# Kernel tuning notes

Measured on AMD Instinct MI355X. Metric: run time of the kernel, lower is better.

Reference implementation:

```python
import math
import jax, jax.numpy as jnp
import numpy as np

SIZE = 1.0            # scene cube extent; positions live in [-SIZE/2, SIZE/2]
N_LEVELS = 16         # number of hash-grid resolutions
TABLE_SIZE = 524288   # 2**19 entries per level
FEAT_DIM = 2          # features per entry
N_POINTS = 262144     # query points (rays * samples)
BASE_RES, MAX_RES = 16, 512

_PRIMES = jnp.array([1, 2654435761, 805459861], dtype=jnp.uint32)
# 8 corner offsets of a voxel, [8,3]
_OFFS = jnp.array([[(c >> 2) & 1, (c >> 1) & 1, c & 1] for c in range(8)], dtype=jnp.uint32)


def _level_lookup(xyz01, table, res):
    # xyz01: [N,3] in [0,1); table: [T,F]; res: scalar int32
    x = xyz01 * res.astype(xyz01.dtype)          # [N,3] grid coords
    x0f = jnp.floor(x)
    w = x - x0f                                  # [N,3] trilinear fracs
    x0 = x0f.astype(jnp.uint32)
    corners = x0[:, None, :] + _OFFS[None]       # [N,8,3]
    h = corners * _PRIMES                        # uint32 wraparound multiply
    idx = (h[..., 0] ^ h[..., 1] ^ h[..., 2]) % jnp.uint32(TABLE_SIZE)  # [N,8]
    feats = table[idx]                           # [N,8,F] gather
    ws = jnp.prod(jnp.where(_OFFS[None] == 1, w[:, None, :], 1.0 - w[:, None, :]), axis=-1)  # [N,8]
    return jnp.einsum('nc,ncf->nf', ws, feats)   # [N,F]


def _forward(xyz, tables, resolutions):
    # xyz: [N,3] in scene coords; tables: [L,T,F]; resolutions: [L] int32
    xyz01 = jnp.clip(xyz / SIZE + 0.5, 0.0, 1.0 - 1e-6)
    per_level = jax.vmap(_level_lookup, in_axes=(None, 0, 0))(xyz01, tables, resolutions)  # [L,N,F]
    return jnp.transpose(per_level, (1, 0, 2)).reshape(xyz.shape[0], N_LEVELS * FEAT_DIM)


def setup_inputs() -> dict:
    key = jax.random.key(0)
    k1, k2 = jax.random.split(key)
    xyz = (jax.random.uniform(k1, (N_POINTS, 3), dtype=jnp.float32) - 0.5) * SIZE
    tables = jax.random.normal(k2, (N_LEVELS, TABLE_SIZE, FEAT_DIM), dtype=jnp.float32) * 1e-2
    growth = (MAX_RES / BASE_RES) ** (1.0 / (N_LEVELS - 1))
    res = np.round(BASE_RES * growth ** np.arange(N_LEVELS)).astype(np.int32)
    return {"xyz": xyz, "tables": tables, "resolutions": jnp.array(res)}


def reference(xyz, tables, resolutions):
    return _forward(xyz, tables, resolutions)
```

## Files before the change

### kernel.cpp

```cpp
#include <hip/hip_runtime.h>


#define HG_N_LEVELS   16
#define HG_TABLE_SIZE 524288u
#define HG_TABLE_MASK (HG_TABLE_SIZE - 1u)

typedef float vf2 __attribute__((ext_vector_type(2)));
typedef float vf4 __attribute__((ext_vector_type(4)));

__device__ __forceinline__ void hg_prep2(
    float px, float py, float pz, float res,
    unsigned* __restrict__ s, float* __restrict__ wyz,
    unsigned* __restrict__ x0out, float* __restrict__ wx)
{
    const float lim = 1.0f - 1e-6f;
    float ux = fminf(fmaxf(px + 0.5f, 0.0f), lim);
    float uy = fminf(fmaxf(py + 0.5f, 0.0f), lim);
    float uz = fminf(fmaxf(pz + 0.5f, 0.0f), lim);
    float fx = ux * res, fy = uy * res, fz = uz * res;
    float x0f = floorf(fx), y0f = floorf(fy), z0f = floorf(fz);
    float wx1 = fx - x0f, wy1 = fy - y0f, wz1 = fz - z0f;
    float wx0 = 1.0f - wx1, wy0 = 1.0f - wy1, wz0 = 1.0f - wz1;
    unsigned x0 = (unsigned)x0f, y0 = (unsigned)y0f, z0 = (unsigned)z0f;
    const unsigned P1 = 2654435761u, P2 = 805459861u;
    unsigned hy0 = y0 * P1, hy1 = (y0 + 1u) * P1;
    unsigned hz0 = z0 * P2, hz1 = (z0 + 1u) * P2;
    s[0] = hy0 ^ hz0;  wyz[0] = wy0 * wz0;
    s[1] = hy0 ^ hz1;  wyz[1] = wy0 * wz1;
    s[2] = hy1 ^ hz0;  wyz[2] = wy1 * wz0;
    s[3] = hy1 ^ hz1;  wyz[3] = wy1 * wz1;
    *x0out = x0; wx[0] = wx0; wx[1] = wx1;
}

__device__ __forceinline__ void hg_prep(
    float px, float py, float pz, float res,
    unsigned* __restrict__ idx, float* __restrict__ w)
{
    unsigned s[4]; float wyz[4], wx[2]; unsigned x0;
    hg_prep2(px, py, pz, res, s, wyz, &x0, wx);
    #pragma unroll
    for (int j = 0; j < 4; ++j) {
        idx[j]     = (x0 ^ s[j]) & HG_TABLE_MASK;        w[j]     = wx[0] * wyz[j];
        idx[4 + j] = ((x0 + 1u) ^ s[j]) & HG_TABLE_MASK; w[4 + j] = wx[1] * wyz[j];
    }
}

__global__ __launch_bounds__(256) void hashgrid_gather_lvl(
    const float* __restrict__ xyz,
    const float* __restrict__ tables,
    const int*   __restrict__ resolutions,
    float*       __restrict__ ws,
    int n_points)
{
    const int x    = blockIdx.x & 7;
    const int slot = blockIdx.x >> 3;
    const int C    = (n_points + 511) >> 9;

    int level, chunk;
    if (slot < C) {
        level = 8 + x; chunk = slot;
    } else {
        int g = ((slot - C) << 3) + x;
        int d = g / C;
        level = 7 - d;
        chunk = g - d * C;
    }
    if (chunk >= C) return;

    const float res = (float)resolutions[level];
    const float2* __restrict__ tbl =
        (const float2*)tables + (size_t)level * HG_TABLE_SIZE;
    float* __restrict__ wlev = ws + (size_t)level * n_points * 2;

    const int p0 = (chunk << 9) + ((int)threadIdx.x << 1);
    if (p0 >= n_points) return;

    if (p0 + 1 < n_points) {
        const float* xp = xyz + (size_t)p0 * 3;
        vf2 c0 = *(const vf2*)(xp);
        vf2 c1 = *(const vf2*)(xp + 2);
        vf2 c2 = *(const vf2*)(xp + 4);

        unsigned sA[4], sB[4], x0A, x0B;
        float wyzA[4], wyzB[4], wxA[2], wxB[2];
        hg_prep2(c0.x, c0.y, c1.x, res, sA, wyzA, &x0A, wxA);
        hg_prep2(c1.y, c2.x, c2.y, res, sB, wyzB, &x0B, wxB);

        unsigned iA0[4], iA1[4], iB0[4], iB1[4];
        #pragma unroll
        for (int j = 0; j < 4; ++j) {
            iA0[j] = (x0A ^ sA[j]) & HG_TABLE_MASK;
            iA1[j] = ((x0A + 1u) ^ sA[j]) & HG_TABLE_MASK;
            iB0[j] = (x0B ^ sB[j]) & HG_TABLE_MASK;
            iB1[j] = ((x0B + 1u) ^ sB[j]) & HG_TABLE_MASK;
        }
        const bool oddA = (x0A & 1u) != 0u;
        const bool oddB = (x0B & 1u) != 0u;

        vf4 qA[4], qB[4];
        #pragma unroll
        for (int j = 0; j < 4; ++j) qA[j] = *(const vf4*)(tbl + (iA0[j] & ~1u));
        #pragma unroll
        for (int j = 0; j < 4; ++j) qB[j] = *(const vf4*)(tbl + (iB0[j] & ~1u));

        vf2 eA[4], eB[4];
        #pragma unroll
        for (int j = 0; j < 4; ++j) { eA[j] = (vf2)(0.f); eB[j] = (vf2)(0.f); }
        if (oddA) {
            #pragma unroll
            for (int j = 0; j < 4; ++j) eA[j] = *(const vf2*)(tbl + iA1[j]);
        }
        if (oddB) {
            #pragma unroll
            for (int j = 0; j < 4; ++j) eB[j] = *(const vf2*)(tbl + iB1[j]);
        }

        asm volatile(""
            : "+v"(qA[0]), "+v"(qA[1]), "+v"(qA[2]), "+v"(qA[3]),
              "+v"(qB[0]), "+v"(qB[1]), "+v"(qB[2]), "+v"(qB[3]),
              "+v"(eA[0]), "+v"(eA[1]), "+v"(eA[2]), "+v"(eA[3]),
              "+v"(eB[0]), "+v"(eB[1]), "+v"(eB[2]), "+v"(eB[3])
            :
            : "memory");

        float oax = 0.f, oay = 0.f, obx = 0.f, oby = 0.f;
        #pragma unroll
        for (int j = 0; j < 4; ++j) {
            bool hi = (iA0[j] & 1u) != 0u;
            vf2 lo;  lo.x  = qA[j].x; lo.y  = qA[j].y;
            vf2 hiv; hiv.x = qA[j].z; hiv.y = qA[j].w;
            vf2 f0 = hi ? hiv : lo;
            vf2 f1 = oddA ? eA[j] : (hi ? lo : hiv);
            float w0 = wxA[0] * wyzA[j], w1 = wxA[1] * wyzA[j];
            oax += w0 * f0.x + w1 * f1.x;
            oay += w0 * f0.y + w1 * f1.y;
        }
        #pragma unroll
        for (int j = 0; j < 4; ++j) {
            bool hi = (iB0[j] & 1u) != 0u;
            vf2 lo;  lo.x  = qB[j].x; lo.y  = qB[j].y;
            vf2 hiv; hiv.x = qB[j].z; hiv.y = qB[j].w;
            vf2 f0 = hi ? hiv : lo;
            vf2 f1 = oddB ? eB[j] : (hi ? lo : hiv);
            float w0 = wxB[0] * wyzB[j], w1 = wxB[1] * wyzB[j];
            obx += w0 * f0.x + w1 * f1.x;
            oby += w0 * f0.y + w1 * f1.y;
        }

        vf4 v; v.x = oax; v.y = oay; v.z = obx; v.w = oby;
        __builtin_nontemporal_store(v, (vf4*)(wlev + 2 * (size_t)p0));
    } else {
        float px = xyz[(size_t)p0 * 3 + 0];
        float py = xyz[(size_t)p0 * 3 + 1];
        float pz = xyz[(size_t)p0 * 3 + 2];
        unsigned idx[8]; float w[8];
        hg_prep(px, py, pz, res, idx, w);
        vf2 f[8];
        #pragma unroll
        for (int k = 0; k < 8; ++k) f[k] = *(const vf2*)(tbl + idx[k]);
        float sx = 0.f, sy = 0.f;
        #pragma unroll
        for (int k = 0; k < 8; ++k) { sx += w[k] * f[k].x; sy += w[k] * f[k].y; }
        vf2 v; v.x = sx; v.y = sy;
        __builtin_nontemporal_store(v, (vf2*)(wlev + 2 * (size_t)p0));
    }
}

#define TP_PTS 256
#define TP_STRIDE (2 * TP_PTS + 4)

__global__ __launch_bounds__(256) void hashgrid_transpose(
    const float* __restrict__ ws,
    float*       __restrict__ out,
    int n_points)
{
    __shared__ float tile[16 * TP_STRIDE];
    const int p0 = blockIdx.x * TP_PTS;
    const int t  = (int)threadIdx.x;
    const int npts = min(TP_PTS, n_points - p0);

    #pragma unroll
    for (int it = 0; it < 8; ++it) {
        int r  = it * 2 + (t >> 7);
        int q  = t & 127;
        int pt = q * 2;
        if (pt < npts) {
            const float* src = ws + (size_t)r * n_points * 2 + (size_t)(p0 + pt) * 2;
            vf4 v;
            if (pt + 1 < npts) v = *(const vf4*)src;
            else { vf2 v2 = *(const vf2*)src; v.x = v2.x; v.y = v2.y; v.z = 0.f; v.w = 0.f; }
            *(vf4*)&tile[r * TP_STRIDE + 4 * q] = v;
        }
    }
    __syncthreads();

    #pragma unroll
    for (int it = 0; it < 8; ++it) {
        int linear = it * 256 + t;
        int pt = linear >> 3;
        int v4 = linear & 7;
        if (pt < npts) {
            vf4 v;
            #pragma unroll
            for (int k = 0; k < 4; ++k) {
                int e = 4 * v4 + k;
                int lev = e >> 1, f = e & 1;
                v[k] = tile[lev * TP_STRIDE + 2 * pt + f];
            }
            __builtin_nontemporal_store(
                v, (vf4*)(out + (size_t)(p0 + pt) * 32 + 4 * v4));
        }
    }
}

__global__ __launch_bounds__(256) void hashgrid_fwd(
    const float* __restrict__ xyz,
    const float* __restrict__ tables,
    const int*   __restrict__ resolutions,
    float*       __restrict__ out,
    int n_points)
{
    int tid   = blockIdx.x * blockDim.x + threadIdx.x;
    int point = tid >> 4;
    int level = tid & 15;
    if (point >= n_points) return;

    float px = xyz[point * 3 + 0];
    float py = xyz[point * 3 + 1];
    float pz = xyz[point * 3 + 2];
    float res = (float)resolutions[level];
    const float2* __restrict__ tbl =
        (const float2*)tables + (size_t)level * HG_TABLE_SIZE;

    unsigned idx[8]; float w[8];
    hg_prep(px, py, pz, res, idx, w);
    vf2 f[8];
    #pragma unroll
    for (int k = 0; k < 8; ++k) f[k] = *(const vf2*)(tbl + idx[k]);
    float ox = 0.f, oy = 0.f;
    #pragma unroll
    for (int k = 0; k < 8; ++k) { ox += w[k] * f[k].x; oy += w[k] * f[k].y; }
    vf2 v; v.x = ox; v.y = oy;
    *(vf2*)(out + (size_t)point * 32 + 2 * level) = v;
}

extern "C" void kernel_launch(void* const* d_in, const int* in_sizes, int n_in,
                              void* d_out, int out_size, void* d_ws, size_t ws_size,
                              hipStream_t stream) {
    const float* xyz         = (const float*)d_in[0];
    const float* tables      = (const float*)d_in[1];
    const int*   resolutions = (const int*)d_in[2];
    float*       out         = (float*)d_out;

    int n_points = in_sizes[0] / 3;
    size_t ws_needed = (size_t)n_points * HG_N_LEVELS * sizeof(float2);

    if (ws_size >= ws_needed) {
        float* ws = (float*)d_ws;
        int C = (n_points + 511) >> 9;
        int slots = 2 * C;
        hashgrid_gather_lvl<<<8 * slots, 256, 0, stream>>>(
            xyz, tables, resolutions, ws, n_points);
        int tblocks = (n_points + TP_PTS - 1) / TP_PTS;
        hashgrid_transpose<<<tblocks, 256, 0, stream>>>(ws, out, n_points);
    } else {
        int n_threads = n_points * HG_N_LEVELS;
        hashgrid_fwd<<<(n_threads + 255) / 256, 256, 0, stream>>>(
            xyz, tables, resolutions, out, n_points);
    }
}
```

Baseline: 205.9 us.

## Merge the six coarsest levels into one block loop and stage xyz in LDS

The gather kernel now gives levels 8-15 and levels 7 and 6 one block per chunk as before. Levels 0-5 are handled by a single block per chunk that loops over those six levels, reusing the loaded coordinates. Coarse-level tables are small and cache-resident, so combining them cuts block count and repeated xyz loads. xyz for each chunk is staged through shared memory with coalesced vf4 loads. The risk is load imbalance, since the merged blocks run six times longer, plus an extra __syncthreads per block.

```diff
diff --git a/kernel.cpp b/kernel.cpp
--- a/kernel.cpp
+++ b/kernel.cpp
@@ -45,6 +45,96 @@
     }
 }
 
+__device__ __forceinline__ vf2 hg_gather1(
+    const float2* __restrict__ tbl, float res,
+    float px, float py, float pz)
+{
+    unsigned idx[8]; float w[8];
+    hg_prep(px, py, pz, res, idx, w);
+    vf2 f[8];
+    #pragma unroll
+    for (int k = 0; k < 8; ++k) f[k] = *(const vf2*)(tbl + idx[k]);
+    float sx = 0.f, sy = 0.f;
+    #pragma unroll
+    for (int k = 0; k < 8; ++k) { sx += w[k] * f[k].x; sy += w[k] * f[k].y; }
+    vf2 v; v.x = sx; v.y = sy;
+    return v;
+}
+
+__device__ __forceinline__ vf4 hg_gather2(
+    const float2* __restrict__ tbl, float res,
+    float ax, float ay, float az, float bx, float by, float bz)
+{
+    unsigned sA[4], sB[4], x0A, x0B;
+    float wyzA[4], wyzB[4], wxA[2], wxB[2];
+    hg_prep2(ax, ay, az, res, sA, wyzA, &x0A, wxA);
+    hg_prep2(bx, by, bz, res, sB, wyzB, &x0B, wxB);
+
+    unsigned iA0[4], iA1[4], iB0[4], iB1[4];
+    #pragma unroll
+    for (int j = 0; j < 4; ++j) {
+        iA0[j] = (x0A ^ sA[j]) & HG_TABLE_MASK;
+        iA1[j] = ((x0A + 1u) ^ sA[j]) & HG_TABLE_MASK;
+        iB0[j] = (x0B ^ sB[j]) & HG_TABLE_MASK;
+        iB1[j] = ((x0B + 1u) ^ sB[j]) & HG_TABLE_MASK;
+    }
+    const bool oddA = (x0A & 1u) != 0u;
+    const bool oddB = (x0B & 1u) != 0u;
+
+    vf4 qA[4], qB[4];
+    #pragma unroll
+    for (int j = 0; j < 4; ++j) qA[j] = *(const vf4*)(tbl + (iA0[j] & ~1u));
+    #pragma unroll
+    for (int j = 0; j < 4; ++j) qB[j] = *(const vf4*)(tbl + (iB0[j] & ~1u));
+
+    vf2 eA[4], eB[4];
+    #pragma unroll
+    for (int j = 0; j < 4; ++j) { eA[j] = (vf2)(0.f); eB[j] = (vf2)(0.f); }
+    if (oddA) {
+        #pragma unroll
+        for (int j = 0; j < 4; ++j) eA[j] = *(const vf2*)(tbl + iA1[j]);
+    }
+    if (oddB) {
+        #pragma unroll
+        for (int j = 0; j < 4; ++j) eB[j] = *(const vf2*)(tbl + iB1[j]);
+    }
+
+    asm volatile(""
+        : "+v"(qA[0]), "+v"(qA[1]), "+v"(qA[2]), "+v"(qA[3]),
+          "+v"(qB[0]), "+v"(qB[1]), "+v"(qB[2]), "+v"(qB[3]),
+          "+v"(eA[0]), "+v"(eA[1]), "+v"(eA[2]), "+v"(eA[3]),
+          "+v"(eB[0]), "+v"(eB[1]), "+v"(eB[2]), "+v"(eB[3])
+        :
+        : "memory");
+
+    float oax = 0.f, oay = 0.f, obx = 0.f, oby = 0.f;
+    #pragma unroll
+    for (int j = 0; j < 4; ++j) {
+        bool hi = (iA0[j] & 1u) != 0u;
+        vf2 lo;  lo.x  = qA[j].x; lo.y  = qA[j].y;
+        vf2 hiv; hiv.x = qA[j].z; hiv.y = qA[j].w;
+        vf2 f0 = hi ? hiv : lo;
+        vf2 f1 = oddA ? eA[j] : (hi ? lo : hiv);
+        float w0 = wxA[0] * wyzA[j], w1 = wxA[1] * wyzA[j];
+        oax += w0 * f0.x + w1 * f1.x;
+        oay += w0 * f0.y + w1 * f1.y;
+    }
+    #pragma unroll
+    for (int j = 0; j < 4; ++j) {
+        bool hi = (iB0[j] & 1u) != 0u;
+        vf2 lo;  lo.x  = qB[j].x; lo.y  = qB[j].y;
+        vf2 hiv; hiv.x = qB[j].z; hiv.y = qB[j].w;
+        vf2 f0 = hi ? hiv : lo;
+        vf2 f1 = oddB ? eB[j] : (hi ? lo : hiv);
+        float w0 = wxB[0] * wyzB[j], w1 = wxB[1] * wyzB[j];
+        obx += w0 * f0.x + w1 * f1.x;
+        oby += w0 * f0.y + w1 * f1.y;
+    }
+
+    vf4 r; r.x = oax; r.y = oay; r.z = obx; r.w = oby;
+    return r;
+}
+
 __global__ __launch_bounds__(256) void hashgrid_gather_lvl(
     const float* __restrict__ xyz,
     const float* __restrict__ tables,
@@ -56,113 +146,89 @@
     const int slot = blockIdx.x >> 3;
     const int C    = (n_points + 511) >> 9;
 
-    int level, chunk;
+    int kind = 0;
+    int level = 0, chunk;
     if (slot < C) {
         level = 8 + x; chunk = slot;
     } else {
         int g = ((slot - C) << 3) + x;
+        if (g >= 3 * C) return;
         int d = g / C;
-        level = 7 - d;
         chunk = g - d * C;
-    }
-    if (chunk >= C) return;
-
-    const float res = (float)resolutions[level];
-    const float2* __restrict__ tbl =
-        (const float2*)tables + (size_t)level * HG_TABLE_SIZE;
-    float* __restrict__ wlev = ws + (size_t)level * n_points * 2;
-
-    const int p0 = (chunk << 9) + ((int)threadIdx.x << 1);
-    if (p0 >= n_points) return;
-
-    if (p0 + 1 < n_points) {
-        const float* xp = xyz + (size_t)p0 * 3;
-        vf2 c0 = *(const vf2*)(xp);
-        vf2 c1 = *(const vf2*)(xp + 2);
-        vf2 c2 = *(const vf2*)(xp + 4);
-
-        unsigned sA[4], sB[4], x0A, x0B;
-        float wyzA[4], wyzB[4], wxA[2], wxB[2];
-        hg_prep2(c0.x, c0.y, c1.x, res, sA, wyzA, &x0A, wxA);
-        hg_prep2(c1.y, c2.x, c2.y, res, sB, wyzB, &x0B, wxB);
-
-        unsigned iA0[4], iA1[4], iB0[4], iB1[4];
-        #pragma unroll
-        for (int j = 0; j < 4; ++j) {
-            iA0[j] = (x0A ^ sA[j]) & HG_TABLE_MASK;
-            iA1[j] = ((x0A + 1u) ^ sA[j]) & HG_TABLE_MASK;
-            iB0[j] = (x0B ^ sB[j]) & HG_TABLE_MASK;
-            iB1[j] = ((x0B + 1u) ^ sB[j]) & HG_TABLE_MASK;
+        if (d == 0)      level = 7;
+        else if (d == 1) level = 6;
+        else             kind = 1;
+    }
+
+    const int base = chunk << 9;
+    if (base >= n_points) return;
+    const int t = (int)threadIdx.x;
+
+    __shared__ float sxyz[1536];
+    const bool full = (base + 512 <= n_points);
+    if (full) {
+        const vf4* __restrict__ src = (const vf4*)(xyz + (size_t)base * 3);
+        vf4* dst = (vf4*)sxyz;
+        dst[t] = src[t];
+        if (t < 128) dst[256 + t] = src[256 + t];
+        __syncthreads();
+    }
+
+    if (kind == 0) {
+        const float res = (float)resolutions[level];
+        const float2* __restrict__ tbl =
+            (const float2*)tables + (size_t)level * HG_TABLE_SIZE;
+        float* __restrict__ wlev = ws + (size_t)level * n_points * 2;
+
+        if (full) {
+            const float* lp = sxyz + 6 * t;
+            vf2 c0 = *(const vf2*)(lp);
+            vf2 c1 = *(const vf2*)(lp + 2);
+            vf2 c2 = *(const vf2*)(lp + 4);
+            const int p0 = base + 2 * t;
+            vf4 v = hg_gather2(tbl, res, c0.x, c0.y, c1.x, c1.y, c2.x, c2.y);
+            __builtin_nontemporal_store(v, (vf4*)(wlev + 2 * (size_t)p0));
+        } else {
+            for (int p = base + t; p < n_points; p += 256) {
+                vf2 v = hg_gather1(tbl, res,
+                                   xyz[(size_t)p * 3 + 0],
+                                   xyz[(size_t)p * 3 + 1],
+                                   xyz[(size_t)p * 3 + 2]);
+                __builtin_nontemporal_store(v, (vf2*)(wlev + 2 * (size_t)p));
+            }
         }
-        const bool oddA = (x0A & 1u) != 0u;
-        const bool oddB = (x0B & 1u) != 0u;
-
-        vf4 qA[4], qB[4];
-        #pragma unroll
-        for (int j = 0; j < 4; ++j) qA[j] = *(const vf4*)(tbl + (iA0[j] & ~1u));
-        #pragma unroll
-        for (int j = 0; j < 4; ++j) qB[j] = *(const vf4*)(tbl + (iB0[j] & ~1u));
-
-        vf2 eA[4], eB[4];
-        #pragma unroll
-        for (int j = 0; j < 4; ++j) { eA[j] = (vf2)(0.f); eB[j] = (vf2)(0.f); }
-        if (oddA) {
-            #pragma unroll
-            for (int j = 0; j < 4; ++j) eA[j] = *(const vf2*)(tbl + iA1[j]);
+    } else {
+        if (full) {
+            const float* lp = sxyz + 6 * t;
+            vf2 c0 = *(const vf2*)(lp);
+            vf2 c1 = *(const vf2*)(lp + 2);
+            vf2 c2 = *(const vf2*)(lp + 4);
+            const int p0 = base + 2 * t;
+            #pragma unroll 1
+            for (int lev = 0; lev < 6; ++lev) {
+                const float res = (float)resolutions[lev];
+                const float2* __restrict__ tbl =
+                    (const float2*)tables + (size_t)lev * HG_TABLE_SIZE;
+                float* __restrict__ wlev = ws + (size_t)lev * n_points * 2;
+                vf4 v = hg_gather2(tbl, res, c0.x, c0.y, c1.x, c1.y, c2.x, c2.y);
+                __builtin_nontemporal_store(v, (vf4*)(wlev + 2 * (size_t)p0));
+            }
+        } else {
+            #pragma unroll 1
+            for (int lev = 0; lev < 6; ++lev) {
+                const float res = (float)resolutions[lev];
+                const float2* __restrict__ tbl =
+                    (const float2*)tables + (size_t)lev * HG_TABLE_SIZE;
+                float* __restrict__ wlev = ws + (size_t)lev * n_points * 2;
+                for (int p = base + t; p < n_points; p += 256) {
+                    vf2 v = hg_gather1(tbl, res,
+                                       xyz[(size_t)p * 3 + 0],
+                                       xyz[(size_t)p * 3 + 1],
+                                       xyz[(size_t)p * 3 + 2]);
+                    __builtin_nontemporal_store(v, (vf2*)(wlev + 2 * (size_t)p));
+                }
+            }
         }
-        if (oddB) {
-            #pragma unroll
-            for (int j = 0; j < 4; ++j) eB[j] = *(const vf2*)(tbl + iB1[j]);
-        }
-
-        asm volatile(""
-            : "+v"(qA[0]), "+v"(qA[1]), "+v"(qA[2]), "+v"(qA[3]),
-              "+v"(qB[0]), "+v"(qB[1]), "+v"(qB[2]), "+v"(qB[3]),
-              "+v"(eA[0]), "+v"(eA[1]), "+v"(eA[2]), "+v"(eA[3]),
-              "+v"(eB[0]), "+v"(eB[1]), "+v"(eB[2]), "+v"(eB[3])
-            :
-            : "memory");
-
-        float oax = 0.f, oay = 0.f, obx = 0.f, oby = 0.f;
-        #pragma unroll
-        for (int j = 0; j < 4; ++j) {
-            bool hi = (iA0[j] & 1u) != 0u;
-            vf2 lo;  lo.x  = qA[j].x; lo.y  = qA[j].y;
-            vf2 hiv; hiv.x = qA[j].z; hiv.y = qA[j].w;
-            vf2 f0 = hi ? hiv : lo;
-            vf2 f1 = oddA ? eA[j] : (hi ? lo : hiv);
-            float w0 = wxA[0] * wyzA[j], w1 = wxA[1] * wyzA[j];
-            oax += w0 * f0.x + w1 * f1.x;
-            oay += w0 * f0.y + w1 * f1.y;
-        }
-        #pragma unroll
-        for (int j = 0; j < 4; ++j) {
-            bool hi = (iB0[j] & 1u) != 0u;
-            vf2 lo;  lo.x  = qB[j].x; lo.y  = qB[j].y;
-            vf2 hiv; hiv.x = qB[j].z; hiv.y = qB[j].w;
-            vf2 f0 = hi ? hiv : lo;
-            vf2 f1 = oddB ? eB[j] : (hi ? lo : hiv);
-            float w0 = wxB[0] * wyzB[j], w1 = wxB[1] * wyzB[j];
-            obx += w0 * f0.x + w1 * f1.x;
-            oby += w0 * f0.y + w1 * f1.y;
-        }
-
-        vf4 v; v.x = oax; v.y = oay; v.z = obx; v.w = oby;
-        __builtin_nontemporal_store(v, (vf4*)(wlev + 2 * (size_t)p0));
-    } else {
-        float px = xyz[(size_t)p0 * 3 + 0];
-        float py = xyz[(size_t)p0 * 3 + 1];
-        float pz = xyz[(size_t)p0 * 3 + 2];
-        unsigned idx[8]; float w[8];
-        hg_prep(px, py, pz, res, idx, w);
-        vf2 f[8];
-        #pragma unroll
-        for (int k = 0; k < 8; ++k) f[k] = *(const vf2*)(tbl + idx[k]);
-        float sx = 0.f, sy = 0.f;
-        #pragma unroll
-        for (int k = 0; k < 8; ++k) { sx += w[k] * f[k].x; sy += w[k] * f[k].y; }
-        vf2 v; v.x = sx; v.y = sy;
-        __builtin_nontemporal_store(v, (vf2*)(wlev + 2 * (size_t)p0));
     }
 }
 
@@ -232,15 +298,7 @@
     const float2* __restrict__ tbl =
         (const float2*)tables + (size_t)level * HG_TABLE_SIZE;
 
-    unsigned idx[8]; float w[8];
-    hg_prep(px, py, pz, res, idx, w);
-    vf2 f[8];
-    #pragma unroll
-    for (int k = 0; k < 8; ++k) f[k] = *(const vf2*)(tbl + idx[k]);
-    float ox = 0.f, oy = 0.f;
-    #pragma unroll
-    for (int k = 0; k < 8; ++k) { ox += w[k] * f[k].x; oy += w[k] * f[k].y; }
-    vf2 v; v.x = ox; v.y = oy;
+    vf2 v = hg_gather1(tbl, res, px, py, pz);
     *(vf2*)(out + (size_t)point * 32 + 2 * level) = v;
 }
 
@@ -257,8 +315,9 @@
 
     if (ws_size >= ws_needed) {
         float* ws = (float*)d_ws;
-        int C = (n_points + 511) >> 9;
-        int slots = 2 * C;
+        int C  = (n_points + 511) >> 9;
+        int S2 = (3 * C + 7) >> 3;
+        int slots = C + S2;
         hashgrid_gather_lvl<<<8 * slots, 256, 0, stream>>>(
             xyz, tables, resolutions, ws, n_points);
         int tblocks = (n_points + TP_PTS - 1) / TP_PTS;
```

New measurement: 212.0 us. +2.9%, slower.

## Move coarse-level gathers into transpose kernel, shrink gather grid to fine levels

Applied to the files above, without the earlier changes.

The six coarsest levels (0-5) are no longer gathered in the first kernel. The transpose kernel now computes them directly: it stages xyz in shared memory, gathers each coarse level with paired 16-byte loads, and writes the results into the shared tile. This removes the workspace writes and reads for those levels and shrinks the first kernel's grid to cover only levels 6-15. The cost is a heavier, serialized per-thread loop in the finalize kernel, which may lengthen its tail.

```diff
diff --git a/kernel.cpp b/kernel.cpp
--- a/kernel.cpp
+++ b/kernel.cpp
@@ -45,7 +45,69 @@
     }
 }
 
-__global__ __launch_bounds__(256) void hashgrid_gather_lvl(
+__device__ __forceinline__ vf2 hg_gather1(
+    const float2* __restrict__ tbl, float res,
+    float px, float py, float pz)
+{
+    unsigned idx[8]; float w[8];
+    hg_prep(px, py, pz, res, idx, w);
+    vf2 f[8];
+    #pragma unroll
+    for (int k = 0; k < 8; ++k) f[k] = *(const vf2*)(tbl + idx[k]);
+    float sx = 0.f, sy = 0.f;
+    #pragma unroll
+    for (int k = 0; k < 8; ++k) { sx += w[k] * f[k].x; sy += w[k] * f[k].y; }
+    vf2 v; v.x = sx; v.y = sy;
+    return v;
+}
+
+__device__ __forceinline__ vf2 hg_gather1p(
+    const float2* __restrict__ tbl, float res,
+    float px, float py, float pz)
+{
+    unsigned s[4], x0; float wyz[4], wx[2];
+    hg_prep2(px, py, pz, res, s, wyz, &x0, wx);
+    unsigned i0[4], i1[4];
+    #pragma unroll
+    for (int j = 0; j < 4; ++j) {
+        i0[j] = (x0 ^ s[j]) & HG_TABLE_MASK;
+        i1[j] = ((x0 + 1u) ^ s[j]) & HG_TABLE_MASK;
+    }
+    const bool odd = (x0 & 1u) != 0u;
+
+    vf4 q[4];
+    #pragma unroll
+    for (int j = 0; j < 4; ++j) q[j] = *(const vf4*)(tbl + (i0[j] & ~1u));
+    vf2 e[4];
+    #pragma unroll
+    for (int j = 0; j < 4; ++j) e[j] = (vf2)(0.f);
+    if (odd) {
+        #pragma unroll
+        for (int j = 0; j < 4; ++j) e[j] = *(const vf2*)(tbl + i1[j]);
+    }
+    asm volatile(""
+        : "+v"(q[0]), "+v"(q[1]), "+v"(q[2]), "+v"(q[3]),
+          "+v"(e[0]), "+v"(e[1]), "+v"(e[2]), "+v"(e[3])
+        :
+        : "memory");
+
+    float ox = 0.f, oy = 0.f;
+    #pragma unroll
+    for (int j = 0; j < 4; ++j) {
+        bool hi = (i0[j] & 1u) != 0u;
+        vf2 lo;  lo.x  = q[j].x; lo.y  = q[j].y;
+        vf2 hiv; hiv.x = q[j].z; hiv.y = q[j].w;
+        vf2 f0 = hi ? hiv : lo;
+        vf2 f1 = odd ? e[j] : (hi ? lo : hiv);
+        float w0 = wx[0] * wyz[j], w1 = wx[1] * wyz[j];
+        ox += w0 * f0.x + w1 * f1.x;
+        oy += w0 * f0.y + w1 * f1.y;
+    }
+    vf2 r; r.x = ox; r.y = oy;
+    return r;
+}
+
+__global__ __launch_bounds__(256) void hashgrid_gather_hard(
     const float* __restrict__ xyz,
     const float* __restrict__ tables,
     const int*   __restrict__ resolutions,
@@ -61,6 +123,7 @@
         level = 8 + x; chunk = slot;
     } else {
         int g = ((slot - C) << 3) + x;
+        if (g >= 2 * C) return;
         int d = g / C;
         level = 7 - d;
         chunk = g - d * C;
@@ -153,15 +216,7 @@
         float px = xyz[(size_t)p0 * 3 + 0];
         float py = xyz[(size_t)p0 * 3 + 1];
         float pz = xyz[(size_t)p0 * 3 + 2];
-        unsigned idx[8]; float w[8];
-        hg_prep(px, py, pz, res, idx, w);
-        vf2 f[8];
-        #pragma unroll
-        for (int k = 0; k < 8; ++k) f[k] = *(const vf2*)(tbl + idx[k]);
-        float sx = 0.f, sy = 0.f;
-        #pragma unroll
-        for (int k = 0; k < 8; ++k) { sx += w[k] * f[k].x; sy += w[k] * f[k].y; }
-        vf2 v; v.x = sx; v.y = sy;
+        vf2 v = hg_gather1(tbl, res, px, py, pz);
         __builtin_nontemporal_store(v, (vf2*)(wlev + 2 * (size_t)p0));
     }
 }
@@ -169,27 +224,60 @@
 #define TP_PTS 256
 #define TP_STRIDE (2 * TP_PTS + 4)
 
-__global__ __launch_bounds__(256) void hashgrid_transpose(
+__global__ __launch_bounds__(256) void hashgrid_finalize(
+    const float* __restrict__ xyz,
+    const float* __restrict__ tables,
+    const int*   __restrict__ resolutions,
     const float* __restrict__ ws,
     float*       __restrict__ out,
     int n_points)
 {
     __shared__ float tile[16 * TP_STRIDE];
+    __shared__ float sxyz[3 * TP_PTS];
     const int p0 = blockIdx.x * TP_PTS;
     const int t  = (int)threadIdx.x;
     const int npts = min(TP_PTS, n_points - p0);
-
-    #pragma unroll
-    for (int it = 0; it < 8; ++it) {
-        int r  = it * 2 + (t >> 7);
-        int q  = t & 127;
-        int pt = q * 2;
+    const bool full = (npts == TP_PTS);
+
+    if (full) {
+        const vf4* __restrict__ src = (const vf4*)(xyz + (size_t)p0 * 3);
+        if (t < 192) ((vf4*)sxyz)[t] = src[t];
+    } else {
+        for (int p = t; p < npts; p += 256) {
+            sxyz[3 * p + 0] = xyz[(size_t)(p0 + p) * 3 + 0];
+            sxyz[3 * p + 1] = xyz[(size_t)(p0 + p) * 3 + 1];
+            sxyz[3 * p + 2] = xyz[(size_t)(p0 + p) * 3 + 2];
+        }
+    }
+
+    #pragma unroll
+    for (int k = 0; k < 5; ++k) {
+        int idx = t + k * 256;
+        int r   = 6 + (idx >> 7);
+        int q   = idx & 127;
+        int pt  = q * 2;
         if (pt < npts) {
             const float* src = ws + (size_t)r * n_points * 2 + (size_t)(p0 + pt) * 2;
             vf4 v;
-            if (pt + 1 < npts) v = *(const vf4*)src;
-            else { vf2 v2 = *(const vf2*)src; v.x = v2.x; v.y = v2.y; v.z = 0.f; v.w = 0.f; }
+            if (pt + 1 < npts) v = __builtin_nontemporal_load((const vf4*)src);
+            else { vf2 v2 = __builtin_nontemporal_load((const vf2*)src);
+                   v.x = v2.x; v.y = v2.y; v.z = 0.f; v.w = 0.f; }
             *(vf4*)&tile[r * TP_STRIDE + 4 * q] = v;
+        }
+    }
+    __syncthreads();
+
+    if (t < npts) {
+        float px = sxyz[3 * t + 0];
+        float py = sxyz[3 * t + 1];
+        float pz = sxyz[3 * t + 2];
+        #pragma unroll 1
+        for (int lev = 0; lev < 6; ++lev) {
+            const float res = (float)resolutions[lev];
+            const float2* __restrict__ tbl =
+                (const float2*)tables + (size_t)lev * HG_TABLE_SIZE;
+            vf2 r = hg_gather1p(tbl, res, px, py, pz);
+            *(vf2*)&tile[lev * TP_STRIDE + 2 * t] = r;
         }
     }
     __syncthreads();
@@ -232,15 +320,7 @@
     const float2* __restrict__ tbl =
         (const float2*)tables + (size_t)level * HG_TABLE_SIZE;
 
-    unsigned idx[8]; float w[8];
-    hg_prep(px, py, pz, res, idx, w);
-    vf2 f[8];
-    #pragma unroll
-    for (int k = 0; k < 8; ++k) f[k] = *(const vf2*)(tbl + idx[k]);
-    float ox = 0.f, oy = 0.f;
-    #pragma unroll
-    for (int k = 0; k < 8; ++k) { ox += w[k] * f[k].x; oy += w[k] * f[k].y; }
-    vf2 v; v.x = ox; v.y = oy;
+    vf2 v = hg_gather1(tbl, res, px, py, pz);
     *(vf2*)(out + (size_t)point * 32 + 2 * level) = v;
 }
 
@@ -257,12 +337,14 @@
 
     if (ws_size >= ws_needed) {
         float* ws = (float*)d_ws;
-        int C = (n_points + 511) >> 9;
-        int slots = 2 * C;
-        hashgrid_gather_lvl<<<8 * slots, 256, 0, stream>>>(
+        int C  = (n_points + 511) >> 9;
+        int S2 = (2 * C + 7) >> 3;
+        int slots = C + S2;
+        hashgrid_gather_hard<<<8 * slots, 256, 0, stream>>>(
             xyz, tables, resolutions, ws, n_points);
-        int tblocks = (n_points + TP_PTS - 1) / TP_PTS;
-        hashgrid_transpose<<<tblocks, 256, 0, stream>>>(ws, out, n_points);
+        int fblocks = (n_points + TP_PTS - 1) / TP_PTS;
+        hashgrid_finalize<<<fblocks, 256, 0, stream>>>(
+            xyz, tables, resolutions, ws, out, n_points);
     } else {
         int n_threads = n_points * HG_N_LEVELS;
         hashgrid_fwd<<<(n_threads + 255) / 256, 256, 0, stream>>>(
```

Result: no change. 204.5 us (-0.7%).
